# Optimization experiments

Measured on AMD Instinct MI355X. Metric: run time of the kernel, lower is better.

Reference implementation:

```python
import jax, jax.numpy as jnp
import numpy as np

D_MODEL = 1024
N_HEADS = 16
D_K = D_MODEL // N_HEADS
SEQ = 2048
BATCH = 4


def setup_inputs() -> dict:
    key = jax.random.key(0)
    ks = jax.random.split(key, 11)
    s = 0.02
    inp = {
        'query': jax.random.normal(ks[0], (SEQ, BATCH, D_MODEL), jnp.float32),
        'key': jax.random.normal(ks[1], (SEQ, BATCH, D_MODEL), jnp.float32),
        'value': jax.random.normal(ks[2], (SEQ, BATCH, D_MODEL), jnp.float32),
        'Wq': jax.random.normal(ks[3], (D_MODEL, D_MODEL), jnp.float32) * s,
        'bq': jnp.zeros((D_MODEL,), jnp.float32),
        'Wk': jax.random.normal(ks[4], (D_MODEL, D_MODEL), jnp.float32) * s,
        'bk': jnp.zeros((D_MODEL,), jnp.float32),
        'Wv': jax.random.normal(ks[5], (D_MODEL, D_MODEL), jnp.float32) * s,
        'bv': jnp.zeros((D_MODEL,), jnp.float32),
        'Wo': jax.random.normal(ks[6], (D_MODEL, D_MODEL), jnp.float32) * s,
        'bo': jnp.zeros((D_MODEL,), jnp.float32),
    }
    return inp


def reference(query, key, value, Wq, bq, Wk, bk, Wv, bv, Wo, bo):
    # inputs are [S, B, D]; module transposes to batch-first
    q_in = jnp.swapaxes(query, 0, 1)  # [B, S, D]
    k_in = jnp.swapaxes(key, 0, 1)
    v_in = jnp.swapaxes(value, 0, 1)
    B, S, _ = q_in.shape
    # torch Linear: x @ W.T + b
    q = (q_in @ Wq.T + bq).reshape(B, S, N_HEADS, D_K)
    k = (k_in @ Wk.T + bk).reshape(B, S, N_HEADS, D_K)
    v = (v_in @ Wv.T + bv).reshape(B, S, N_HEADS, D_K)
    scale = jnp.sqrt(jnp.float32(D_K))
    scores = jnp.einsum('bqhd,bkhd->bhqk', q, k) / scale  # [B, H, S, S]
    attn = jax.nn.softmax(scores, axis=-1)
    # dropout is identity in eval / p=0
    context = jnp.einsum('bhqk,bkhd->bqhd', attn, v).reshape(B, S, D_MODEL)
    out = context @ Wo.T + bo  # [B, S, D]
    return jnp.swapaxes(out, 0, 1)  # back to [S, B, D]
```

## Files before the change

kernel.cpp:

```cpp
#include <hip/hip_runtime.h>
#include <math.h>

typedef unsigned short u16;
typedef unsigned int   u32;
typedef float f32x4  __attribute__((ext_vector_type(4)));
typedef float f32x16 __attribute__((ext_vector_type(16)));
typedef __bf16 bf16x8 __attribute__((ext_vector_type(8)));
typedef __bf16 bf16x2 __attribute__((ext_vector_type(2)));

#define SEQ   2048
#define BATCH 4
#define NH    16
#define DK    64
#define DM    1024
#define MTOT  (SEQ*BATCH)
#define SCL_QK 0.18033688011116016f

#if __has_builtin(__builtin_amdgcn_exp2f)
#define EXP2(x) __builtin_amdgcn_exp2f(x)
#else
#define EXP2(x) exp2f(x)
#endif

static __device__ __forceinline__ u16 f2bf(float f) {
  __bf16 h = (__bf16)f;
  return __builtin_bit_cast(u16, h);
}
static __device__ __forceinline__ u32 pk2(float a, float b) {
  bf16x2 t = {(__bf16)a, (__bf16)b};
  return __builtin_bit_cast(u32, t);
}

typedef __attribute__((address_space(1))) const void g1_t;
typedef __attribute__((address_space(3))) void l3_t;
static __device__ __forceinline__ void gload16(const void* g, void* l) {
  __builtin_amdgcn_global_load_lds((g1_t*)g, (l3_t*)l, 16, 0, 0);
}

static __device__ __forceinline__ void cast8(const float* __restrict__ src,
                                             u16* __restrict__ dst, int i) {
  float4 a = ((const float4*)src)[2 * i];
  float4 b = ((const float4*)src)[2 * i + 1];
  uint4 r;
  r.x = pk2(a.x, a.y); r.y = pk2(a.z, a.w);
  r.z = pk2(b.x, b.y); r.w = pk2(b.z, b.w);
  ((uint4*)dst)[i] = r;
}

__global__ __launch_bounds__(256)
void cast_bf16(const float* __restrict__ src, u16* __restrict__ dst, int n8) {
  int i = blockIdx.x * 256 + threadIdx.x;
  if (i < n8) cast8(src, dst, i);
}

__global__ __launch_bounds__(256)
void cast_w(const float* __restrict__ Wq, const float* __restrict__ Wk,
            const float* __restrict__ Wv, const float* __restrict__ Wo,
            u16* __restrict__ w3, u16* __restrict__ wo_c) {
  int bid = blockIdx.x;
  int t = bid >> 9, idx = bid & 511;
  const float* src = (t == 0) ? Wq : (t == 1) ? Wk : (t == 2) ? Wv : Wo;
  u16* dst = (t < 3) ? (w3 + (size_t)t * DM * DM) : wo_c;
  cast8(src, dst, idx * 256 + threadIdx.x);
}

__global__ __launch_bounds__(256)
void cast_all(const float* __restrict__ q, const float* __restrict__ k,
              const float* __restrict__ v,
              const float* __restrict__ Wq, const float* __restrict__ Wk,
              const float* __restrict__ Wv, const float* __restrict__ Wo,
              u16* __restrict__ in_c, u16* __restrict__ w3, u16* __restrict__ wo_c) {
  int bid = blockIdx.x;
  const float* src; u16* dst; int idx;
  if (bid < 12288) {
    int t = bid >> 12; idx = bid & 4095;
    src = (t == 0) ? q : (t == 1) ? k : v;
    dst = in_c + (size_t)t * MTOT * DM;
  } else {
    int wb = bid - 12288;
    int t = wb >> 9; idx = wb & 511;
    src = (t == 0) ? Wq : (t == 1) ? Wk : (t == 2) ? Wv : Wo;
    dst = (t < 3) ? (w3 + (size_t)t * DM * DM) : wo_c;
  }
  cast8(src, dst, idx * 256 + threadIdx.x);
}

template<int OGEMM>
__global__ __launch_bounds__(256, 4)
void gemm_k(const u16* __restrict__ a0, const u16* __restrict__ a1,
            const u16* __restrict__ a2, const u16* __restrict__ w3,
            const float* __restrict__ b0, const float* __restrict__ b1,
            const float* __restrict__ b2,
            u16* __restrict__ o0, u16* __restrict__ o1, u16* __restrict__ o2,
            float* __restrict__ o3, int seg_base)
{
  constexpr int BM = 128, BN = 128, BK = 32;
  __shared__ u16 As[2][BM * BK];
  __shared__ u16 Bs[2][BN * BK];

  const int nwg = gridDim.x * gridDim.y;
  const int bid = blockIdx.y * gridDim.x + blockIdx.x;
  const int swz = (bid & 7) * (nwg >> 3) + (bid >> 3);
  const int bx  = swz % gridDim.x;
  const int by  = swz / gridDim.x;

  const int seg = OGEMM ? 0 : (seg_base + (bx >> 3));
  const int n0  = OGEMM ? bx * BN : (bx & 7) * BN;
  const int m0  = by * BM;
  const u16* A = OGEMM ? a0 : (seg == 0 ? a0 : seg == 1 ? a1 : a2);
  const u16* W = OGEMM ? w3 : (w3 + (size_t)seg * DM * DM);
  const float* bias = OGEMM ? b0 : (seg == 0 ? b0 : seg == 1 ? b1 : b2);

  const int tid  = threadIdx.x;
  const int w    = tid >> 6;
  const int lane = tid & 63;
  const int quad = lane >> 4;
  const int l15  = lane & 15;
  const int wm = (w >> 1) * 64;
  const int wn = (w & 1) * 64;

  size_t aoff[2], woff[2];
  for (int p = 0; p < 2; p++) {
    int row = w * 32 + p * 16 + (lane >> 2);
    int gm = m0 + row;
    if (OGEMM) {
      aoff[p] = (size_t)gm * DM + (lane & 3) * 8;
    } else {
      int bb = gm >> 11, s = gm & (SEQ - 1);
      aoff[p] = (size_t)(s * BATCH + bb) * DM + (lane & 3) * 8;
    }
    woff[p] = (size_t)(n0 + row) * DM + (lane & 3) * 8;
  }

  f32x4 zero4 = {0.f, 0.f, 0.f, 0.f};
  f32x4 acc[4][4];
  for (int i = 0; i < 4; i++)
    for (int j = 0; j < 4; j++)
      acc[i][j] = zero4;

#pragma unroll
  for (int p = 0; p < 2; p++) {
    gload16(A + aoff[p], &As[0][(w * 32 + p * 16) * BK]);
    gload16(W + woff[p], &Bs[0][(w * 32 + p * 16) * BK]);
  }
  __syncthreads();

  constexpr int NKT = DM / BK;
  for (int kt = 0; kt < NKT; kt++) {
    const int cur = kt & 1;
    if (kt + 1 < NKT) {
      const int nk = (kt + 1) * BK;
#pragma unroll
      for (int p = 0; p < 2; p++) {
        gload16(A + aoff[p] + nk, &As[cur ^ 1][(w * 32 + p * 16) * BK]);
        gload16(W + woff[p] + nk, &Bs[cur ^ 1][(w * 32 + p * 16) * BK]);
      }
    }
    bf16x8 af[4], bfr[4];
#pragma unroll
    for (int i = 0; i < 4; i++)
      af[i] = *(const bf16x8*)&As[cur][(wm + i * 16 + l15) * BK + quad * 8];
#pragma unroll
    for (int j = 0; j < 4; j++)
      bfr[j] = *(const bf16x8*)&Bs[cur][(wn + j * 16 + l15) * BK + quad * 8];
#pragma unroll
    for (int i = 0; i < 4; i++)
#pragma unroll
      for (int j = 0; j < 4; j++)
        acc[i][j] = __builtin_amdgcn_mfma_f32_16x16x32_bf16(af[i], bfr[j], acc[i][j], 0, 0, 0);
    __syncthreads();
  }

  for (int j = 0; j < 4; j++) {
    int gn = n0 + wn + j * 16 + l15;
    float bv = bias[gn];
    int h = gn >> 6, dk = gn & 63;
    for (int i = 0; i < 4; i++) {
      int gmb = m0 + wm + i * 16 + quad * 4;
      for (int r = 0; r < 4; r++) {
        int gm = gmb + r;
        float val = acc[i][j][r] + bv;
        int bb = gm >> 11, s = gm & (SEQ - 1);
        if (OGEMM) {
          o3[(size_t)(s * BATCH + bb) * DM + gn] = val;
        } else if (seg == 0) {
          o0[((size_t)(bb * NH + h) * SEQ + s) * DK + dk] = f2bf(val * SCL_QK);
        } else if (seg == 1) {
          o1[((size_t)(bb * NH + h) * SEQ + s) * DK + dk] = f2bf(val);
        } else {
          o2[((size_t)(bb * NH + h) * DK + dk) * SEQ + s] = f2bf(val);
        }
      }
    }
  }
}

__global__ __launch_bounds__(256, 4)
void attn3(const u16* __restrict__ Q, const u16* __restrict__ K,
           const u16* __restrict__ VT, u16* __restrict__ ctx)
{
  __shared__ u16 Ks[2][64 * 64];
  __shared__ u16 Vs[2][64 * 64];

  const int bh = blockIdx.x;
  const int qt = blockIdx.y;
  const int b  = bh >> 4, h = bh & 15;
  const int tid  = threadIdx.x;
  const int w    = tid >> 6;
  const int lane = tid & 63;
  const int l31  = lane & 31;
  const int hi   = lane >> 5;

  const u16* Qb = Q  + (size_t)bh * SEQ * DK;
  const u16* Kb = K  + (size_t)bh * SEQ * DK;
  const u16* Vb = VT + (size_t)bh * DK * SEQ;

  const int qbase = qt * 128 + w * 32;
  const int qrow  = qbase + l31;

  bf16x8 qf[4];
#pragma unroll
  for (int ks = 0; ks < 4; ks++)
    qf[ks] = *(const bf16x8*)&Qb[(size_t)qrow * DK + ks * 16 + hi * 8];

  const int r0 = tid >> 3;
  const int sw = (tid & 7) ^ (r0 & 7);

#define STAGE(kbb, bufi) do {                                                       \
    _Pragma("unroll")                                                               \
    for (int p = 0; p < 2; p++) {                                                   \
      int row = p * 32 + r0;                                                        \
      gload16(&Kb[(size_t)((kbb) * 64 + row) * DK + sw * 8],                        \
              &Ks[bufi][(p * 32 + w * 8) * 64]);                                    \
      gload16(&Vb[(size_t)row * SEQ + (kbb) * 64 + sw * 8],                         \
              &Vs[bufi][(p * 32 + w * 8) * 64]);                                    \
    }                                                                               \
  } while (0)

  f32x16 z16;
#pragma unroll
  for (int i = 0; i < 16; i++) z16[i] = 0.f;

  f32x16 ot0 = z16, ot1 = z16;
  float2 ls2 = {0.f, 0.f};

  STAGE(0, 0);
  __syncthreads();

  for (int kb = 0; kb < SEQ / 64; kb++) {
    const int buf = kb & 1;
    if (kb + 1 < SEQ / 64) STAGE(kb + 1, buf ^ 1);

    const u16* KsB = &Ks[buf][0];
    const u16* VsB = &Vs[buf][0];

    f32x16 sa0 = z16, sa1 = z16;
#pragma unroll
    for (int ks = 0; ks < 4; ks++) {
      const int g0 = ((ks * 2 + hi) ^ (l31 & 7)) * 8;
      bf16x8 kf0 = *(const bf16x8*)&KsB[l31 * 64 + g0];
      bf16x8 kf1 = *(const bf16x8*)&KsB[(32 + l31) * 64 + g0];
      sa0 = __builtin_amdgcn_mfma_f32_32x32x16_bf16(kf0, qf[ks], sa0, 0, 0, 0);
      sa1 = __builtin_amdgcn_mfma_f32_32x32x16_bf16(kf1, qf[ks], sa1, 0, 0, 0);
    }

    u32 wp[8];

#define SOFTMAX_BLK(SA) do {                                                        \
    _Pragma("unroll")                                                               \
    for (int g = 0; g < 8; g++) {                                                   \
      float pa = EXP2(SA[2 * g]);                                                   \
      float pb = EXP2(SA[2 * g + 1]);                                               \
      ls2.x += pa; ls2.y += pb;                                                     \
      wp[g] = pk2(pa, pb);                                                          \
    }                                                                               \
  } while (0)

#define PVSTEP(KSB, KSL) do {                                                       \
    u32 a0 = wp[(KSB) * 4 + 0], a1 = wp[(KSB) * 4 + 1];                             \
    u32 a2 = wp[(KSB) * 4 + 2], a3 = wp[(KSB) * 4 + 3];                             \
    u32 s0 = hi ? a0 : a2, s1 = hi ? a1 : a3;                                       \
    u32 x0 = (u32)__shfl_xor((int)s0, 32);                                          \
    u32 x1 = (u32)__shfl_xor((int)s1, 32);                                          \
    uint4 pw;                                                                       \
    pw.x = hi ? x0 : a0; pw.y = hi ? x1 : a1;                                       \
    pw.z = hi ? a2 : x0; pw.w = hi ? a3 : x1;                                       \
    bf16x8 pf = __builtin_bit_cast(bf16x8, pw);                                     \
    const int gg = (((KSL) * 2 + hi) ^ (l31 & 7)) * 8;                              \
    bf16x8 vf0 = *(const bf16x8*)&VsB[l31 * 64 + gg];                               \
    bf16x8 vf1 = *(const bf16x8*)&VsB[(32 + l31) * 64 + gg];                        \
    ot0 = __builtin_amdgcn_mfma_f32_32x32x16_bf16(vf0, pf, ot0, 0, 0, 0);           \
    ot1 = __builtin_amdgcn_mfma_f32_32x32x16_bf16(vf1, pf, ot1, 0, 0, 0);           \
  } while (0)

    SOFTMAX_BLK(sa0);
    PVSTEP(0, 0);
    PVSTEP(1, 1);
    SOFTMAX_BLK(sa1);
    PVSTEP(0, 2);
    PVSTEP(1, 3);

    __syncthreads();
  }

  float ls = ls2.x + ls2.y;
  ls += __shfl_xor(ls, 32);
  float inv = 1.0f / ls;

  u16* crow = ctx + ((size_t)(b * SEQ + qrow)) * DM + h * DK;

#define STORE_BLK(OT, DKB) do {                                                     \
    _Pragma("unroll")                                                               \
    for (int t = 0; t < 4; t++) {                                                   \
      uint2 pr;                                                                     \
      pr.x = pk2(OT[4 * t + 0] * inv, OT[4 * t + 1] * inv);                         \
      pr.y = pk2(OT[4 * t + 2] * inv, OT[4 * t + 3] * inv);                         \
      *(uint2*)&crow[(DKB) * 32 + t * 8 + hi * 4] = pr;                             \
    }                                                                               \
  } while (0)

  STORE_BLK(ot0, 0);
  STORE_BLK(ot1, 1);

#undef STAGE
#undef SOFTMAX_BLK
#undef PVSTEP
#undef STORE_BLK
}

extern "C" void kernel_launch(void* const* d_in, const int* in_sizes, int n_in,
                              void* d_out, int out_size, void* d_ws, size_t ws_size,
                              hipStream_t stream)
{
  const float* q  = (const float*)d_in[0];
  const float* k  = (const float*)d_in[1];
  const float* v  = (const float*)d_in[2];
  const float* Wq = (const float*)d_in[3];
  const float* bq = (const float*)d_in[4];
  const float* Wk = (const float*)d_in[5];
  const float* bk = (const float*)d_in[6];
  const float* Wv = (const float*)d_in[7];
  const float* bv = (const float*)d_in[8];
  const float* Wo = (const float*)d_in[9];
  const float* bo = (const float*)d_in[10];

  const size_t SZ_IN  = (size_t)MTOT * DM;
  const size_t SZ_W   = (size_t)DM * DM;
  const size_t NEED_FUSED = (3 * SZ_IN + 3 * SZ_W + SZ_W + 3 * SZ_IN) * 2;

  dim3 cblk(256);
  dim3 ggq(24, 64);
  dim3 ggs(8, 64);

  if (ws_size >= NEED_FUSED) {
    u16* in_c  = (u16*)d_ws;
    u16* w3    = in_c + 3 * SZ_IN;
    u16* wo_c  = w3   + 3 * SZ_W;
    u16* q_ws  = wo_c + SZ_W;
    u16* k_ws  = q_ws + SZ_IN;
    u16* vt_ws = k_ws + SZ_IN;
    u16* ctx   = in_c;

    cast_all<<<14336, cblk, 0, stream>>>(q, k, v, Wq, Wk, Wv, Wo, in_c, w3, wo_c);
    gemm_k<0><<<ggq, cblk, 0, stream>>>(in_c, in_c + SZ_IN, in_c + 2 * SZ_IN, w3,
                                        bq, bk, bv, q_ws, k_ws, vt_ws, nullptr, 0);
    attn3<<<dim3(BATCH * NH, SEQ / 128), cblk, 0, stream>>>(q_ws, k_ws, vt_ws, ctx);
    gemm_k<1><<<ggs, cblk, 0, stream>>>(ctx, ctx, ctx, wo_c,
                                        bo, bo, bo, nullptr, nullptr, nullptr,
                                        (float*)d_out, 0);
  } else {
    u16* in_c  = (u16*)d_ws;
    u16* w3    = in_c + SZ_IN;
    u16* wo_c  = w3   + 3 * SZ_W;
    u16* q_ws  = wo_c + SZ_W;
    u16* k_ws  = q_ws + SZ_IN;
    u16* vt_ws = k_ws + SZ_IN;
    u16* ctx   = in_c;

    const int NA8 = MTOT * DM / 8;
    cast_w<<<2048, cblk, 0, stream>>>(Wq, Wk, Wv, Wo, w3, wo_c);
    cast_bf16<<<NA8 / 256, cblk, 0, stream>>>(q, in_c, NA8);
    gemm_k<0><<<ggs, cblk, 0, stream>>>(in_c, in_c, in_c, w3, bq, bk, bv,
                                        q_ws, k_ws, vt_ws, nullptr, 0);
    cast_bf16<<<NA8 / 256, cblk, 0, stream>>>(k, in_c, NA8);
    gemm_k<0><<<ggs, cblk, 0, stream>>>(in_c, in_c, in_c, w3, bq, bk, bv,
                                        q_ws, k_ws, vt_ws, nullptr, 1);
    cast_bf16<<<NA8 / 256, cblk, 0, stream>>>(v, in_c, NA8);
    gemm_k<0><<<ggs, cblk, 0, stream>>>(in_c, in_c, in_c, w3, bq, bk, bv,
                                        q_ws, k_ws, vt_ws, nullptr, 2);
    attn3<<<dim3(BATCH * NH, SEQ / 128), cblk, 0, stream>>>(q_ws, k_ws, vt_ws, ctx);
    gemm_k<1><<<ggs, cblk, 0, stream>>>(ctx, ctx, ctx, wo_c,
                                        bo, bo, bo, nullptr, nullptr, nullptr,
                                        (float*)d_out, 0);
  }
}
```

Measured before the change: 360.7 us.

## Triple-buffer LDS staging with vmcnt waits in GEMM and attention loops

```diff
diff --git a/kernel.cpp b/kernel.cpp
--- a/kernel.cpp
+++ b/kernel.cpp
@@ -21,6 +21,12 @@
 #else
 #define EXP2(x) exp2f(x)
 #endif
+
+#define WAITCNT_VM(N) asm volatile("s_waitcnt vmcnt(" #N ")" ::: "memory")
+#define BARRIER_FENCED() do {                                  \
+    __builtin_amdgcn_s_barrier();                              \
+    asm volatile("" ::: "memory");                             \
+  } while (0)
 
 static __device__ __forceinline__ u16 f2bf(float f) {
   __bf16 h = (__bf16)f;
@@ -95,8 +101,8 @@
             float* __restrict__ o3, int seg_base)
 {
   constexpr int BM = 128, BN = 128, BK = 32;
-  __shared__ u16 As[2][BM * BK];
-  __shared__ u16 Bs[2][BN * BK];
+  __shared__ u16 As[3][BM * BK];
+  __shared__ u16 Bs[3][BN * BK];
 
   const int nwg = gridDim.x * gridDim.y;
   const int bid = blockIdx.y * gridDim.x + blockIdx.x;
@@ -138,24 +144,14 @@
     for (int j = 0; j < 4; j++)
       acc[i][j] = zero4;
 
-#pragma unroll
-  for (int p = 0; p < 2; p++) {
-    gload16(A + aoff[p], &As[0][(w * 32 + p * 16) * BK]);
-    gload16(W + woff[p], &Bs[0][(w * 32 + p * 16) * BK]);
-  }
-  __syncthreads();
-
-  constexpr int NKT = DM / BK;
-  for (int kt = 0; kt < NKT; kt++) {
-    const int cur = kt & 1;
-    if (kt + 1 < NKT) {
-      const int nk = (kt + 1) * BK;
-#pragma unroll
-      for (int p = 0; p < 2; p++) {
-        gload16(A + aoff[p] + nk, &As[cur ^ 1][(w * 32 + p * 16) * BK]);
-        gload16(W + woff[p] + nk, &Bs[cur ^ 1][(w * 32 + p * 16) * BK]);
-      }
+  auto stage = [&](int kt, int bufi) {
+#pragma unroll
+    for (int p = 0; p < 2; p++) {
+      gload16(A + aoff[p] + kt * BK, &As[bufi][(w * 32 + p * 16) * BK]);
+      gload16(W + woff[p] + kt * BK, &Bs[bufi][(w * 32 + p * 16) * BK]);
     }
+  };
+  auto compute = [&](int cur) {
     bf16x8 af[4], bfr[4];
 #pragma unroll
     for (int i = 0; i < 4; i++)
@@ -168,8 +164,25 @@
 #pragma unroll
       for (int j = 0; j < 4; j++)
         acc[i][j] = __builtin_amdgcn_mfma_f32_16x16x32_bf16(af[i], bfr[j], acc[i][j], 0, 0, 0);
-    __syncthreads();
-  }
+  };
+
+  constexpr int NKT = DM / BK;
+  stage(0, 0);
+  stage(1, 1);
+  int cur = 0;
+  for (int kt = 0; kt < NKT - 1; kt++) {
+    WAITCNT_VM(4);
+    BARRIER_FENCED();
+    compute(cur);
+    if (kt + 2 < NKT) {
+      int nb = cur + 2; if (nb >= 3) nb -= 3;
+      stage(kt + 2, nb);
+    }
+    cur = (cur + 1 == 3) ? 0 : cur + 1;
+  }
+  WAITCNT_VM(0);
+  BARRIER_FENCED();
+  compute(cur);
 
   for (int j = 0; j < 4; j++) {
     int gn = n0 + wn + j * 16 + l15;
@@ -199,8 +212,8 @@
 void attn3(const u16* __restrict__ Q, const u16* __restrict__ K,
            const u16* __restrict__ VT, u16* __restrict__ ctx)
 {
-  __shared__ u16 Ks[2][64 * 64];
-  __shared__ u16 Vs[2][64 * 64];
+  __shared__ u16 Ks[3][64 * 64];
+  __shared__ u16 Vs[3][64 * 64];
 
   const int bh = blockIdx.x;
   const int qt = blockIdx.y;
@@ -244,27 +257,7 @@
   f32x16 ot0 = z16, ot1 = z16;
   float2 ls2 = {0.f, 0.f};
 
-  STAGE(0, 0);
-  __syncthreads();
-
-  for (int kb = 0; kb < SEQ / 64; kb++) {
-    const int buf = kb & 1;
-    if (kb + 1 < SEQ / 64) STAGE(kb + 1, buf ^ 1);
-
-    const u16* KsB = &Ks[buf][0];
-    const u16* VsB = &Vs[buf][0];
-
-    f32x16 sa0 = z16, sa1 = z16;
-#pragma unroll
-    for (int ks = 0; ks < 4; ks++) {
-      const int g0 = ((ks * 2 + hi) ^ (l31 & 7)) * 8;
-      bf16x8 kf0 = *(const bf16x8*)&KsB[l31 * 64 + g0];
-      bf16x8 kf1 = *(const bf16x8*)&KsB[(32 + l31) * 64 + g0];
-      sa0 = __builtin_amdgcn_mfma_f32_32x32x16_bf16(kf0, qf[ks], sa0, 0, 0, 0);
-      sa1 = __builtin_amdgcn_mfma_f32_32x32x16_bf16(kf1, qf[ks], sa1, 0, 0, 0);
-    }
-
-    u32 wp[8];
+  u32 wp[8];
 
 #define SOFTMAX_BLK(SA) do {                                                        \
     _Pragma("unroll")                                                               \
@@ -276,7 +269,7 @@
     }                                                                               \
   } while (0)
 
-#define PVSTEP(KSB, KSL) do {                                                       \
+#define PVSTEP(VsB, KSB, KSL) do {                                                  \
     u32 a0 = wp[(KSB) * 4 + 0], a1 = wp[(KSB) * 4 + 1];                             \
     u32 a2 = wp[(KSB) * 4 + 2], a3 = wp[(KSB) * 4 + 3];                             \
     u32 s0 = hi ? a0 : a2, s1 = hi ? a1 : a3;                                       \
@@ -293,15 +286,43 @@
     ot1 = __builtin_amdgcn_mfma_f32_32x32x16_bf16(vf1, pf, ot1, 0, 0, 0);           \
   } while (0)
 
-    SOFTMAX_BLK(sa0);
-    PVSTEP(0, 0);
-    PVSTEP(1, 1);
-    SOFTMAX_BLK(sa1);
-    PVSTEP(0, 2);
-    PVSTEP(1, 3);
-
-    __syncthreads();
-  }
+#define BODY(curi) do {                                                             \
+    const u16* KsB = &Ks[curi][0];                                                  \
+    const u16* VsB = &Vs[curi][0];                                                  \
+    f32x16 sa0 = z16, sa1 = z16;                                                    \
+    _Pragma("unroll")                                                               \
+    for (int ks = 0; ks < 4; ks++) {                                                \
+      const int g0 = ((ks * 2 + hi) ^ (l31 & 7)) * 8;                               \
+      bf16x8 kf0 = *(const bf16x8*)&KsB[l31 * 64 + g0];                             \
+      bf16x8 kf1 = *(const bf16x8*)&KsB[(32 + l31) * 64 + g0];                      \
+      sa0 = __builtin_amdgcn_mfma_f32_32x32x16_bf16(kf0, qf[ks], sa0, 0, 0, 0);     \
+      sa1 = __builtin_amdgcn_mfma_f32_32x32x16_bf16(kf1, qf[ks], sa1, 0, 0, 0);     \
+    }                                                                               \
+    SOFTMAX_BLK(sa0);                                                               \
+    PVSTEP(VsB, 0, 0);                                                              \
+    PVSTEP(VsB, 1, 1);                                                              \
+    SOFTMAX_BLK(sa1);                                                               \
+    PVSTEP(VsB, 0, 2);                                                              \
+    PVSTEP(VsB, 1, 3);                                                              \
+  } while (0)
+
+  constexpr int NKB = SEQ / 64;
+  STAGE(0, 0);
+  STAGE(1, 1);
+  int cur = 0;
+  for (int kb = 0; kb < NKB - 1; kb++) {
+    WAITCNT_VM(4);
+    BARRIER_FENCED();
+    BODY(cur);
+    if (kb + 2 < NKB) {
+      int nb = cur + 2; if (nb >= 3) nb -= 3;
+      STAGE(kb + 2, nb);
+    }
+    cur = (cur + 1 == 3) ? 0 : cur + 1;
+  }
+  WAITCNT_VM(0);
+  BARRIER_FENCED();
+  BODY(cur);
 
   float ls = ls2.x + ls2.y;
   ls += __shfl_xor(ls, 32);
@@ -325,6 +346,7 @@
 #undef STAGE
 #undef SOFTMAX_BLK
 #undef PVSTEP
+#undef BODY
 #undef STORE_BLK
 }
 
```

After: 372.9 us. 1.03x slower.
